# Performance work log

Hardware: AMD Instinct MI355X
Metric: run time of the kernel (lower is better)

The kernel has to match this reference:

```python
import jax, jax.numpy as jnp
import numpy as np

SQRT_DIM = np.sqrt(64.0).astype(np.float32)
NEG_INF = -1000000000.0


def setup_inputs() -> dict:
    key = jax.random.key(0)
    kq, kk, kv = jax.random.split(key, 3)
    B, H, S, D = 4, 8, 2048, 64
    q = jax.random.normal(kq, (B, H, S, D), dtype=jnp.float32)
    k = jax.random.normal(kk, (B, H, S, D), dtype=jnp.float32)
    v = jax.random.normal(kv, (B, H, S, D), dtype=jnp.float32)
    mask = jnp.ones((B, 1, S, S), dtype=jnp.int32)
    return {"q": q, "k": k, "v": v, "mask": mask}


def reference(q, k, v, mask):
    # scores: [B, H, S, S]
    attn = jnp.einsum("bhqd,bhkd->bhqk", q, k) / SQRT_DIM
    attn = jnp.where(mask == 0, NEG_INF, attn)
    attn = jax.nn.softmax(attn, axis=-1)
    # dropout p=0.0 -> identity
    output = jnp.einsum("bhqk,bhkd->bhqd", attn, v)
    return (output, attn)
```

## Files before the change

kernel.cpp:

```cpp
#include <hip/hip_runtime.h>
#include <hip/hip_bf16.h>
#include <stdint.h>

#define NB 4
#define NH 8
#define SDIM 2048
#define DDIM 64

#define KSCALE 0.18033688011112042f

typedef short s8v __attribute__((ext_vector_type(8)));
typedef float f4v __attribute__((ext_vector_type(4)));

__device__ __forceinline__ float bf2f(unsigned short h) {
    union { unsigned int u; float f; } c; c.u = ((unsigned int)h) << 16; return c.f;
}
__device__ __forceinline__ unsigned short f2bf(float x) {
    union { float f; unsigned int u; } c; c.f = x;
    return (unsigned short)((c.u + 0x7FFFu + ((c.u >> 16) & 1u)) >> 16);
}

__global__ void sdpa_prep_cast_k(const float* __restrict__ k, unsigned short* __restrict__ kb) {
    int i = blockIdx.x * 256 + threadIdx.x;
    float4 v = ((const float4*)k)[i];
    ushort4 o;
    o.x = f2bf(v.x * KSCALE);
    o.y = f2bf(v.y * KSCALE);
    o.z = f2bf(v.z * KSCALE);
    o.w = f2bf(v.w * KSCALE);
    ((ushort4*)kb)[i] = o;
}

__global__ void sdpa_prep_transpose_v(const float* __restrict__ v, unsigned short* __restrict__ vt) {
    __shared__ float t[64][65];
    const int bh = blockIdx.x >> 5;
    const int kt = blockIdx.x & 31;
    const int tid = threadIdx.x;
    const float* src = v + ((size_t)bh * SDIM + (size_t)kt * 64) * DDIM;
    #pragma unroll
    for (int i = 0; i < 4; ++i) {
        int idx = i * 256 + tid;
        int kl = idx >> 4, c4 = idx & 15;
        float4 val = ((const float4*)(src + kl * DDIM))[c4];
        t[kl][c4 * 4 + 0] = val.x; t[kl][c4 * 4 + 1] = val.y;
        t[kl][c4 * 4 + 2] = val.z; t[kl][c4 * 4 + 3] = val.w;
    }
    __syncthreads();
    const int d   = tid >> 2;
    const int klb = (tid & 3) << 4;
    unsigned short* dst = vt + ((size_t)bh * DDIM + d) * SDIM + kt * 64 + klb;
    #pragma unroll
    for (int c = 0; c < 4; ++c) {
        ushort4 w;
        w.x = f2bf(t[klb + c * 4 + 0][d]);
        w.y = f2bf(t[klb + c * 4 + 1][d]);
        w.z = f2bf(t[klb + c * 4 + 2][d]);
        w.w = f2bf(t[klb + c * 4 + 3][d]);
        ((ushort4*)dst)[c] = w;
    }
}

__launch_bounds__(512, 4)
__global__ void sdpa_main(const float* __restrict__ q,
                          const unsigned short* __restrict__ kb,
                          const unsigned short* __restrict__ vtb,
                          const int* __restrict__ mask,
                          float* __restrict__ outO,
                          float* __restrict__ outP) {
    extern __shared__ char lds[];
    unsigned short* sc = (unsigned short*)lds;

    const int bx = blockIdx.x;
    const int bh = bx >> 7;
    const int q0 = (bx & 127) << 4;
    const int b  = bh >> 3;

    const int tid  = threadIdx.x;
    const int wave = tid >> 6;
    const int lane = tid & 63;
    const int l15  = lane & 15;
    const int quad = lane >> 4;

    s8v aq0, aq1;
    {
        const float* qr = q + ((size_t)bh * SDIM + q0 + l15) * DDIM + quad * 8;
        float4 x0 = ((const float4*)qr)[0];
        float4 x1 = ((const float4*)qr)[1];
        float4 y0 = ((const float4*)(qr + 32))[0];
        float4 y1 = ((const float4*)(qr + 32))[1];
        aq0[0]=(short)f2bf(x0.x); aq0[1]=(short)f2bf(x0.y); aq0[2]=(short)f2bf(x0.z); aq0[3]=(short)f2bf(x0.w);
        aq0[4]=(short)f2bf(x1.x); aq0[5]=(short)f2bf(x1.y); aq0[6]=(short)f2bf(x1.z); aq0[7]=(short)f2bf(x1.w);
        aq1[0]=(short)f2bf(y0.x); aq1[1]=(short)f2bf(y0.y); aq1[2]=(short)f2bf(y0.z); aq1[3]=(short)f2bf(y0.w);
        aq1[4]=(short)f2bf(y1.x); aq1[5]=(short)f2bf(y1.y); aq1[6]=(short)f2bf(y1.z); aq1[7]=(short)f2bf(y1.w);
    }

    {
        const unsigned short* kbase = kb + (size_t)bh * SDIM * DDIM;
        const int n_start = wave << 8;
        #pragma unroll 2
        for (int t = 0; t < 16; ++t) {
            const int n0 = n_start + (t << 4);
            const unsigned short* krow = kbase + (size_t)(n0 + l15) * DDIM + quad * 8;
            s8v b0 = *(const s8v*)(krow);
            s8v b1 = *(const s8v*)(krow + 32);
            f4v acc = {0.f, 0.f, 0.f, 0.f};
            acc = __builtin_amdgcn_mfma_f32_16x16x32_bf16(aq0, b0, acc, 0, 0, 0);
            acc = __builtin_amdgcn_mfma_f32_16x16x32_bf16(aq1, b1, acc, 0, 0, 0);
            const int col = n0 + l15;
            const int blk = col >> 3;
            const int off = col & 7;
            #pragma unroll
            for (int r = 0; r < 4; ++r) {
                int row = quad * 4 + r;
                sc[row * 2048 + (((blk ^ row) << 3) | off)] = f2bf(acc[r]);
            }
        }
    }
    __syncthreads();

    const int row = tid >> 5;
    const int l32 = tid & 31;
    unsigned short* scrow = sc + row * 2048;
    const int* mrow = mask + (size_t)b * SDIM * SDIM + (size_t)(q0 + row) * SDIM;

    float s[64];
    float rmax = -3.0e38f;
    #pragma unroll
    for (int i = 0; i < 8; ++i) {
        const int j = l32 + (i << 5);
        s8v vv = *(const s8v*)(scrow + ((j ^ row) << 3));
        int4 m0 = ((const int4*)mrow)[j * 2 + 0];
        int4 m1 = ((const int4*)mrow)[j * 2 + 1];
        const int mm[8] = { m0.x, m0.y, m0.z, m0.w, m1.x, m1.y, m1.z, m1.w };
        #pragma unroll
        for (int e = 0; e < 8; ++e) {
            float x = bf2f((unsigned short)vv[e]);
            x = (mm[e] == 0) ? -1.0e9f : x;
            s[i * 8 + e] = x;
            rmax = fmaxf(rmax, x);
        }
    }
    #pragma unroll
    for (int d = 1; d < 32; d <<= 1) rmax = fmaxf(rmax, __shfl_xor(rmax, d));

    float rsum = 0.f;
    #pragma unroll
    for (int i = 0; i < 64; ++i) {
        float e = exp2f(s[i] - rmax);
        s[i] = e;
        rsum += e;
    }
    #pragma unroll
    for (int d = 1; d < 32; d <<= 1) rsum += __shfl_xor(rsum, d);
    const float rinv = 1.0f / rsum;

    {
        float* prow = outP + (size_t)bh * SDIM * SDIM + (size_t)(q0 + row) * SDIM;
        #pragma unroll
        for (int i = 0; i < 8; ++i) {
            const int j = l32 + (i << 5);
            float p0 = s[i*8+0] * rinv, p1 = s[i*8+1] * rinv;
            float p2 = s[i*8+2] * rinv, p3 = s[i*8+3] * rinv;
            float p4 = s[i*8+4] * rinv, p5 = s[i*8+5] * rinv;
            float p6 = s[i*8+6] * rinv, p7 = s[i*8+7] * rinv;
            f4v o0 = { p0, p1, p2, p3 };
            f4v o1 = { p4, p5, p6, p7 };
            __builtin_nontemporal_store(o0, (f4v*)prow + j * 2 + 0);
            __builtin_nontemporal_store(o1, (f4v*)prow + j * 2 + 1);
            s8v vv;
            vv[0]=(short)f2bf(p0); vv[1]=(short)f2bf(p1); vv[2]=(short)f2bf(p2); vv[3]=(short)f2bf(p3);
            vv[4]=(short)f2bf(p4); vv[5]=(short)f2bf(p5); vv[6]=(short)f2bf(p6); vv[7]=(short)f2bf(p7);
            *(s8v*)(scrow + ((j ^ row) << 3)) = vv;
        }
    }
    __syncthreads();

    {
        const int dt = wave & 3;
        const int kh = wave >> 2;
        const unsigned short* vbase = vtb + ((size_t)bh * DDIM + (dt << 4) + l15) * SDIM
                                          + (kh << 10) + quad * 8;
        const unsigned short* arow = sc + l15 * 2048;
        f4v acc0 = {0,0,0,0}, acc1 = {0,0,0,0};
        #pragma unroll 4
        for (int ks = 0; ks < 32; ++ks) {
            const int k0 = (kh << 10) + (ks << 5);
            s8v a  = *(const s8v*)(arow + ((((k0 >> 3) + quad) ^ l15) << 3));
            s8v bb = *(const s8v*)(vbase + (ks << 5));
            if (ks & 1) acc1 = __builtin_amdgcn_mfma_f32_16x16x32_bf16(a, bb, acc1, 0, 0, 0);
            else        acc0 = __builtin_amdgcn_mfma_f32_16x16x32_bf16(a, bb, acc0, 0, 0, 0);
        }
        f4v acc = acc0 + acc1;

        __syncthreads();
        float* scratch = (float*)lds;
        if (kh == 1) {
            #pragma unroll
            for (int r = 0; r < 4; ++r)
                scratch[(dt << 8) + ((quad * 4 + r) << 4) + l15] = acc[r];
        }
        __syncthreads();
        if (kh == 0) {
            float* orow = outO + ((size_t)bh * SDIM + q0) * DDIM + (dt << 4) + l15;
            #pragma unroll
            for (int r = 0; r < 4; ++r)
                orow[(quad * 4 + r) * DDIM] = acc[r] + scratch[(dt << 8) + ((quad * 4 + r) << 4) + l15];
        }
    }
}

extern "C" void kernel_launch(void* const* d_in, const int* in_sizes, int n_in,
                              void* d_out, int out_size, void* d_ws, size_t ws_size,
                              hipStream_t stream) {
    const float* q  = (const float*)d_in[0];
    const float* k  = (const float*)d_in[1];
    const float* v  = (const float*)d_in[2];
    const int* mask = (const int*)d_in[3];

    const size_t qkv_elems = (size_t)NB * NH * SDIM * DDIM;
    float* outO = (float*)d_out;
    float* outP = (float*)d_out + qkv_elems;

    unsigned short* kb  = (unsigned short*)d_ws;
    unsigned short* vtb = kb + qkv_elems;

    sdpa_prep_cast_k<<<(int)(qkv_elems / 1024), 256, 0, stream>>>(k, kb);
    sdpa_prep_transpose_v<<<NB * NH * (SDIM / 64), 256, 0, stream>>>(v, vtb);
    sdpa_main<<<NB * NH * (SDIM / 16), 512, 65536, stream>>>(q, kb, vtb, mask, outO, outP);
}
```

Before: 865.2 us.

## Prefetch mask rows before barrier and process softmax one row per wave in two passes

Softmax now assigns one full row per wave, handled in two passes, instead of a row per half-wave. The mask for the first row is loaded before the barrier so it overlaps the QK^T stage. The second row's mask is prefetched while the first row is being processed. This hides global mask load latency at the cost of two serialized passes and 64-lane shuffle reductions, though register pressure drops from 64 to 32 scores plus the prefetched mask.

```diff
diff --git a/kernel.cpp b/kernel.cpp
--- a/kernel.cpp
+++ b/kernel.cpp
@@ -116,61 +116,81 @@
             }
         }
     }
+
+    const int* mbase = mask + (size_t)b * SDIM * SDIM + (size_t)q0 * SDIM;
+    int4 ma[8];
+    {
+        const int4* mrow = (const int4*)(mbase + (size_t)wave * SDIM);
+        #pragma unroll
+        for (int i = 0; i < 4; ++i) {
+            const int blk = lane + (i << 6);
+            ma[2 * i + 0] = mrow[blk * 2 + 0];
+            ma[2 * i + 1] = mrow[blk * 2 + 1];
+        }
+    }
     __syncthreads();
 
-    const int row = tid >> 5;
-    const int l32 = tid & 31;
-    unsigned short* scrow = sc + row * 2048;
-    const int* mrow = mask + (size_t)b * SDIM * SDIM + (size_t)(q0 + row) * SDIM;
-
-    float s[64];
-    float rmax = -3.0e38f;
     #pragma unroll
-    for (int i = 0; i < 8; ++i) {
-        const int j = l32 + (i << 5);
-        s8v vv = *(const s8v*)(scrow + ((j ^ row) << 3));
-        int4 m0 = ((const int4*)mrow)[j * 2 + 0];
-        int4 m1 = ((const int4*)mrow)[j * 2 + 1];
-        const int mm[8] = { m0.x, m0.y, m0.z, m0.w, m1.x, m1.y, m1.z, m1.w };
-        #pragma unroll
-        for (int e = 0; e < 8; ++e) {
-            float x = bf2f((unsigned short)vv[e]);
-            x = (mm[e] == 0) ? -1.0e9f : x;
-            s[i * 8 + e] = x;
-            rmax = fmaxf(rmax, x);
-        }
-    }
-    #pragma unroll
-    for (int d = 1; d < 32; d <<= 1) rmax = fmaxf(rmax, __shfl_xor(rmax, d));
-
-    float rsum = 0.f;
-    #pragma unroll
-    for (int i = 0; i < 64; ++i) {
-        float e = exp2f(s[i] - rmax);
-        s[i] = e;
-        rsum += e;
-    }
-    #pragma unroll
-    for (int d = 1; d < 32; d <<= 1) rsum += __shfl_xor(rsum, d);
-    const float rinv = 1.0f / rsum;
-
-    {
+    for (int pass = 0; pass < 2; ++pass) {
+        const int row = wave + (pass << 3);
+        unsigned short* scrow = sc + row * 2048;
+
+        float s[32];
+        float rmax = -3.0e38f;
+        #pragma unroll
+        for (int i = 0; i < 4; ++i) {
+            const int blk = lane + (i << 6);
+            s8v vv = *(const s8v*)(scrow + ((blk ^ row) << 3));
+            const int4 m0 = ma[2 * i + 0];
+            const int4 m1 = ma[2 * i + 1];
+            const int mm[8] = { m0.x, m0.y, m0.z, m0.w, m1.x, m1.y, m1.z, m1.w };
+            #pragma unroll
+            for (int e = 0; e < 8; ++e) {
+                float x = bf2f((unsigned short)vv[e]);
+                x = (mm[e] == 0) ? -1.0e9f : x;
+                s[i * 8 + e] = x;
+                rmax = fmaxf(rmax, x);
+            }
+        }
+        if (pass == 0) {
+            const int4* mrow = (const int4*)(mbase + (size_t)(wave + 8) * SDIM);
+            #pragma unroll
+            for (int i = 0; i < 4; ++i) {
+                const int blk = lane + (i << 6);
+                ma[2 * i + 0] = mrow[blk * 2 + 0];
+                ma[2 * i + 1] = mrow[blk * 2 + 1];
+            }
+        }
+        #pragma unroll
+        for (int d = 1; d < 64; d <<= 1) rmax = fmaxf(rmax, __shfl_xor(rmax, d));
+
+        float rsum = 0.f;
+        #pragma unroll
+        for (int i = 0; i < 32; ++i) {
+            float e = exp2f(s[i] - rmax);
+            s[i] = e;
+            rsum += e;
+        }
+        #pragma unroll
+        for (int d = 1; d < 64; d <<= 1) rsum += __shfl_xor(rsum, d);
+        const float rinv = 1.0f / rsum;
+
         float* prow = outP + (size_t)bh * SDIM * SDIM + (size_t)(q0 + row) * SDIM;
         #pragma unroll
-        for (int i = 0; i < 8; ++i) {
-            const int j = l32 + (i << 5);
+        for (int i = 0; i < 4; ++i) {
+            const int blk = lane + (i << 6);
             float p0 = s[i*8+0] * rinv, p1 = s[i*8+1] * rinv;
             float p2 = s[i*8+2] * rinv, p3 = s[i*8+3] * rinv;
             float p4 = s[i*8+4] * rinv, p5 = s[i*8+5] * rinv;
             float p6 = s[i*8+6] * rinv, p7 = s[i*8+7] * rinv;
             f4v o0 = { p0, p1, p2, p3 };
             f4v o1 = { p4, p5, p6, p7 };
-            __builtin_nontemporal_store(o0, (f4v*)prow + j * 2 + 0);
-            __builtin_nontemporal_store(o1, (f4v*)prow + j * 2 + 1);
+            __builtin_nontemporal_store(o0, (f4v*)prow + blk * 2 + 0);
+            __builtin_nontemporal_store(o1, (f4v*)prow + blk * 2 + 1);
             s8v vv;
             vv[0]=(short)f2bf(p0); vv[1]=(short)f2bf(p1); vv[2]=(short)f2bf(p2); vv[3]=(short)f2bf(p3);
             vv[4]=(short)f2bf(p4); vv[5]=(short)f2bf(p5); vv[6]=(short)f2bf(p6); vv[7]=(short)f2bf(p7);
-            *(s8v*)(scrow + ((j ^ row) << 3)) = vv;
+            *(s8v*)(scrow + ((blk ^ row) << 3)) = vv;
         }
     }
     __syncthreads();
```

After: 842.8 us. 2.6% less time.
